# Performance work log

Measured on AMD Instinct MI355X. Metric: run time of the kernel, lower is better.

The kernel has to match this reference:

```python
import jax, jax.numpy as jnp
import numpy as np

N = 100000   # nodes
E = 1600000  # directed edges
HID = 64


def gat_conv(x, src, dst, W, a_src, a_dst, b, heads, out_ch):
    """PyG-style GATConv (add_self_loops=True, negative_slope=0.2, concat)."""
    n = x.shape[0]
    h = (x @ W).reshape(n, heads, out_ch)              # [N,H,C]
    loop = jnp.arange(n, dtype=src.dtype)
    s = jnp.concatenate([src, loop])                   # self loops appended
    d = jnp.concatenate([dst, loop])
    alpha_src = jnp.sum(h * a_src, axis=-1)            # [N,H]
    alpha_dst = jnp.sum(h * a_dst, axis=-1)            # [N,H]
    alpha = jax.nn.leaky_relu(alpha_src[s] + alpha_dst[d], 0.2)  # [E+N,H]
    # segment softmax over incoming edges of each destination node
    amax = jax.ops.segment_max(alpha, d, num_segments=n)
    alpha = jnp.exp(alpha - amax[d])
    asum = jax.ops.segment_sum(alpha, d, num_segments=n)
    alpha = alpha / (asum[d] + 1e-16)
    msg = h[s] * alpha[:, :, None]                     # [E+N,H,C]
    out = jax.ops.segment_sum(msg, d, num_segments=n)  # [N,H,C]
    return out.reshape(n, heads * out_ch) + b


def setup_inputs() -> dict:
    key = jax.random.key(0)
    ks = jax.random.split(key, 22)
    rn = lambda k, shp, s=0.1: (jax.random.normal(k, shp, jnp.float32) * s)
    inp = {
        "x": jax.random.normal(ks[0], (N, 2), jnp.float32),
        "edge_index": jax.random.randint(ks[1], (2, E), 0, N, dtype=jnp.int32),
        "edge_attr": jax.random.normal(ks[2], (E, 2), jnp.float32),
        # node encoder
        "enc_W": rn(ks[3], (2, HID)), "enc_b": rn(ks[4], (HID,)),
        # gat1: heads=4, out=16
        "g1_W": rn(ks[5], (HID, HID)), "g1_as": rn(ks[6], (4, 16)),
        "g1_ad": rn(ks[7], (4, 16)), "g1_b": rn(ks[8], (HID,)),
        # gat2: heads=1, out=64
        "g2_W": rn(ks[9], (HID, HID)), "g2_as": rn(ks[10], (1, HID)),
        "g2_ad": rn(ks[11], (1, HID)), "g2_b": rn(ks[12], (HID,)),
        # node head
        "no_W1": rn(ks[13], (HID, HID)), "no_b1": rn(ks[14], (HID,)),
        "no_W2": rn(ks[15], (HID, 2)), "no_b2": rn(ks[16], (2,)),
        # edge head: in = 2*HID + 2 = 130
        "eo_W1": rn(ks[17], (2 * HID + 2, HID)), "eo_b1": rn(ks[18], (HID,)),
        "eo_W2": rn(ks[19], (HID, 1)), "eo_b2": rn(ks[20], (1,)),
    }
    return inp


def reference(x, edge_index, edge_attr, enc_W, enc_b,
              g1_W, g1_as, g1_ad, g1_b,
              g2_W, g2_as, g2_ad, g2_b,
              no_W1, no_b1, no_W2, no_b2,
              eo_W1, eo_b1, eo_W2, eo_b2):
    src, dst = edge_index[0], edge_index[1]
    h = x @ enc_W + enc_b                                    # node encoder (dropout = eval identity)
    h = jax.nn.elu(gat_conv(h, src, dst, g1_W, g1_as, g1_ad, g1_b, 4, 16))
    h = gat_conv(h, src, dst, g2_W, g2_as, g2_ad, g2_b, 1, HID)
    e_in = jnp.concatenate([h[src], h[dst], edge_attr], axis=-1)  # [E,130]
    node_pred = jnp.tanh(jax.nn.leaky_relu(h @ no_W1 + no_b1, 0.01) @ no_W2 + no_b2)
    edge_pred = jnp.tanh(jax.nn.leaky_relu(e_in @ eo_W1 + eo_b1, 0.01) @ eo_W2 + eo_b2)[:, 0]
    return edge_pred, node_pred
```

## Files before the change

### kernel.cpp

```cpp
#include <hip/hip_runtime.h>
#include <hip/hip_fp16.h>
#include <math.h>


typedef _Float16 half8_t __attribute__((ext_vector_type(8)));
typedef float floatx4 __attribute__((ext_vector_type(4)));

__global__ void k_scatter(const int* __restrict__ src, const int* __restrict__ dst,
                          int E, int NB, int cap, int* cursor,
                          unsigned int* __restrict__ ebuf,
                          const float* __restrict__ encW, const float* __restrict__ encb,
                          const float* __restrict__ g1W, float* __restrict__ Mc){
  __shared__ int hist[800];
  __shared__ int base[800];
  int t = threadIdx.x;
  if (blockIdx.x == 0 && t < 64){
    float m0 = 0.f, m1 = 0.f, cc = 0.f;
    for (int k = 0; k < 64; ++k){
      float g = g1W[k * 64 + t];
      m0 = fmaf(encW[k], g, m0);
      m1 = fmaf(encW[64 + k], g, m1);
      cc = fmaf(encb[k], g, cc);
    }
    Mc[t] = m0; Mc[64 + t] = m1; Mc[128 + t] = cc;
  }
  for (int i = t; i < NB; i += 256) hist[i] = 0;
  __syncthreads();
  int cbase = blockIdx.x * 2048;
  int sv[8], bk[8], dl[8];
  #pragma unroll
  for (int i = 0; i < 8; ++i){
    int e = cbase + i * 256 + t;
    if (e < E){
      int d = dst[e];
      sv[i] = src[e]; bk[i] = d >> 7; dl[i] = d & 127;
      atomicAdd(&hist[bk[i]], 1);
    } else bk[i] = -1;
  }
  __syncthreads();
  for (int i = t; i < NB; i += 256){
    int c = hist[i];
    base[i] = (c > 0) ? (i * cap + atomicAdd(&cursor[i], c)) : 0;
    hist[i] = 0;
  }
  __syncthreads();
  #pragma unroll
  for (int i = 0; i < 8; ++i){
    if (bk[i] >= 0){
      int r = atomicAdd(&hist[bk[i]], 1);
      int p = base[bk[i]] + r;
      if (p < (bk[i] + 1) * cap)
        ebuf[p] = (unsigned)sv[i] | ((unsigned)dl[i] << 17);
    }
  }
}

__global__ void k_bucket_build(const int* __restrict__ cursor, int cap, int N,
                               unsigned int* ebuf, int* __restrict__ rstart,
                               int* __restrict__ rend){
  __shared__ unsigned int ent[2700];
  __shared__ int cnts[128];
  __shared__ int aux[128];
  int b = blockIdx.x, t = threadIdx.x;
  int base = b * cap;
  int cnt = cursor[b];
  if (cnt > cap) cnt = cap;
  for (int i = t; i < cnt; i += 256) ent[i] = ebuf[base + i];
  if (t < 128) cnts[t] = 0;
  __syncthreads();
  for (int i = t; i < cnt; i += 256) atomicAdd(&cnts[ent[i] >> 17], 1);
  __syncthreads();
  int v = 0;
  if (t < 128){ v = cnts[t]; aux[t] = v; }
  __syncthreads();
  for (int off = 1; off < 128; off <<= 1){
    int x = 0;
    if (t < 128 && t >= off) x = aux[t - off];
    __syncthreads();
    if (t < 128) aux[t] += x;
    __syncthreads();
  }
  if (t < 128){
    int incl = aux[t];
    int node = (b << 7) + t;
    if (node < N){ rstart[node] = base + incl - v; rend[node] = base + incl; }
    cnts[t] = incl - v;
  }
  __syncthreads();
  for (int i = t; i < cnt; i += 256){
    unsigned int en = ent[i];
    int pos = atomicAdd(&cnts[en >> 17], 1);
    ebuf[base + pos] = en;
  }
}

template<int H>
__global__ void k_palpha(const int* __restrict__ cursor, int cap,
                         const unsigned int* __restrict__ ebuf,
                         const float* __restrict__ as, const float* __restrict__ ad,
                         float* __restrict__ palpha){
  int blk = blockIdx.x;
  int b = blk >> 2, part = blk & 3;
  int base = b * cap;
  int cnt = cursor[b];
  if (cnt > cap) cnt = cap;
  for (int i = part * 256 + threadIdx.x; i < cnt; i += 1024){
    unsigned int en = ebuf[base + i];
    int s = en & 0x1FFFFu;
    int d = (b << 7) + (en >> 17);
    if (H == 4){
      float4 sv = ((const float4*)as)[s];
      float4 dv = ((const float4*)ad)[d];
      float a0 = sv.x + dv.x, a1 = sv.y + dv.y, a2 = sv.z + dv.z, a3 = sv.w + dv.w;
      a0 = a0 > 0.f ? a0 : 0.2f * a0;
      a1 = a1 > 0.f ? a1 : 0.2f * a1;
      a2 = a2 > 0.f ? a2 : 0.2f * a2;
      a3 = a3 > 0.f ? a3 : 0.2f * a3;
      float4 pv = {__expf(a0), __expf(a1), __expf(a2), __expf(a3)};
      ((float4*)palpha)[base + i] = pv;
    } else {
      float a = as[s] + ad[d];
      a = a > 0.f ? a : 0.2f * a;
      palpha[base + i] = __expf(a);
    }
  }
}

__global__ void k_fuse1(const float* __restrict__ x, const float* __restrict__ Mc,
                        const float* __restrict__ a_s, const float* __restrict__ a_d,
                        __half* __restrict__ hw, float* __restrict__ alpha_s,
                        float* __restrict__ alpha_d, int n){
  int idx = blockIdx.x * blockDim.x + threadIdx.x;
  if (idx >= n * 64) return;
  int node = idx >> 6, j = idx & 63;
  float acc = fmaf(x[node * 2 + 0], Mc[j], fmaf(x[node * 2 + 1], Mc[64 + j], Mc[128 + j]));
  hw[idx] = __float2half(acc);
  float ps = acc * a_s[j];
  float pd = acc * a_d[j];
  #pragma unroll
  for (int off = 1; off < 16; off <<= 1){
    ps += __shfl_xor(ps, off);
    pd += __shfl_xor(pd, off);
  }
  if ((j & 15) == 0){
    int h = j >> 4;
    alpha_s[node * 4 + h] = ps;
    alpha_d[node * 4 + h] = pd;
  }
}

__global__ __launch_bounds__(256) void k_hw_mfma(
    const __half* __restrict__ hin, const float* __restrict__ W,
    const float* __restrict__ a_s, const float* __restrict__ a_d,
    __half* __restrict__ hw, float* __restrict__ alpha_s,
    float* __restrict__ alpha_d, int n){
  __shared__ float redS[4][16];
  __shared__ float redD[4][16];
  int t = threadIdx.x;
  int lane = t & 63, wave = t >> 6;
  int l15 = lane & 15, quad = lane >> 4;
  int ch = wave * 16 + l15;
  half8_t b0, b1;
  #pragma unroll
  for (int j = 0; j < 8; ++j){
    b0[j] = (_Float16)W[(quad * 8 + j) * 64 + ch];
    b1[j] = (_Float16)W[(quad * 8 + j + 32) * 64 + ch];
  }
  float asv = a_s[ch], adv = a_d[ch];
  int base = blockIdx.x * 64;
  for (int it = 0; it < 4; ++it){
    int tb = base + it * 16;
    if (tb >= n) break;
    int arn = tb + l15; if (arn >= n) arn = n - 1;
    const __half* arow = hin + (size_t)arn * 64 + quad * 8;
    half8_t a0 = *(const half8_t*)arow;
    half8_t a1 = *(const half8_t*)(arow + 32);
    floatx4 acc = {0.f, 0.f, 0.f, 0.f};
    acc = __builtin_amdgcn_mfma_f32_16x16x32_f16(a0, b0, acc, 0, 0, 0);
    acc = __builtin_amdgcn_mfma_f32_16x16x32_f16(a1, b1, acc, 0, 0, 0);
    float ps[4], pd[4];
    #pragma unroll
    for (int r = 0; r < 4; ++r){
      int node = tb + quad * 4 + r;
      if (node < n) hw[(size_t)node * 64 + ch] = __float2half(acc[r]);
      ps[r] = acc[r] * asv;
      pd[r] = acc[r] * adv;
      #pragma unroll
      for (int off = 1; off < 16; off <<= 1){
        ps[r] += __shfl_xor(ps[r], off);
        pd[r] += __shfl_xor(pd[r], off);
      }
    }
    if (l15 == 0){
      #pragma unroll
      for (int r = 0; r < 4; ++r){
        redS[wave][quad * 4 + r] = ps[r];
        redD[wave][quad * 4 + r] = pd[r];
      }
    }
    __syncthreads();
    if (t < 16 && tb + t < n){
      alpha_s[tb + t] = redS[0][t] + redS[1][t] + redS[2][t] + redS[3][t];
      alpha_d[tb + t] = redD[0][t] + redD[1][t] + redD[2][t] + redD[3][t];
    }
    __syncthreads();
  }
}

template<int H, bool ELU_ACT>
__global__ void k_agg(const __half* __restrict__ hw, const float* __restrict__ palpha,
                      const float* __restrict__ alpha_s, const float* __restrict__ alpha_d,
                      const int* __restrict__ rstart, const int* __restrict__ rend,
                      const unsigned int* __restrict__ ebuf,
                      const float* __restrict__ bias, __half* __restrict__ hout, int n){
  int node = (blockIdx.x * blockDim.x + threadIdx.x) >> 6;
  int lane = threadIdx.x & 63;
  int g = lane >> 3, jj = lane & 7;
  if (node >= n) return;
  int hidx = (jj * H) >> 3;
  int start = rstart[node], end = rend[node];
  float acc[8] = {0.f,0.f,0.f,0.f,0.f,0.f,0.f,0.f};
  float psum = 0.f;
  if (g == 0){
    float a = alpha_s[node * H + hidx] + alpha_d[node * H + hidx];
    a = a > 0.f ? a : 0.2f * a;
    float p = __expf(a);
    psum = p;
    float4 rv = *(const float4*)(hw + (size_t)node * 64 + jj * 8);
    const __half2* hp = (const __half2*)&rv;
    #pragma unroll
    for (int k = 0; k < 4; ++k){
      float2 f = __half22float2(hp[k]);
      acc[2 * k] = p * f.x; acc[2 * k + 1] = p * f.y;
    }
  }
  int i = start + g;
  for (; i + 8 < end; i += 16){
    unsigned int e0 = ebuf[i], e1 = ebuf[i + 8];
    int s0 = e0 & 0x1FFFF, s1 = e1 & 0x1FFFF;
    float p0 = palpha[(size_t)i * H + hidx];
    float p1 = palpha[(size_t)(i + 8) * H + hidx];
    float4 r0 = *(const float4*)(hw + (size_t)s0 * 64 + jj * 8);
    float4 r1 = *(const float4*)(hw + (size_t)s1 * 64 + jj * 8);
    const __half2* h0 = (const __half2*)&r0;
    const __half2* h1 = (const __half2*)&r1;
    psum += p0 + p1;
    #pragma unroll
    for (int k = 0; k < 4; ++k){
      float2 f0 = __half22float2(h0[k]);
      float2 f1 = __half22float2(h1[k]);
      acc[2 * k]     = fmaf(p0, f0.x, fmaf(p1, f1.x, acc[2 * k]));
      acc[2 * k + 1] = fmaf(p0, f0.y, fmaf(p1, f1.y, acc[2 * k + 1]));
    }
  }
  if (i < end){
    unsigned int en = ebuf[i];
    int s = en & 0x1FFFF;
    float p = palpha[(size_t)i * H + hidx];
    float4 rv = *(const float4*)(hw + (size_t)s * 64 + jj * 8);
    const __half2* hp = (const __half2*)&rv;
    psum += p;
    #pragma unroll
    for (int k = 0; k < 4; ++k){
      float2 f = __half22float2(hp[k]);
      acc[2 * k]     = fmaf(p, f.x, acc[2 * k]);
      acc[2 * k + 1] = fmaf(p, f.y, acc[2 * k + 1]);
    }
  }
  #pragma unroll
  for (int off = 8; off < 64; off <<= 1){
    psum += __shfl_xor(psum, off);
    #pragma unroll
    for (int k = 0; k < 8; ++k) acc[k] += __shfl_xor(acc[k], off);
  }
  if (g == 0){
    float inv = 1.f / (psum + 1e-16f);
    float4 bv0 = ((const float4*)bias)[2 * jj];
    float4 bv1 = ((const float4*)bias)[2 * jj + 1];
    float o[8];
    o[0] = fmaf(acc[0], inv, bv0.x); o[1] = fmaf(acc[1], inv, bv0.y);
    o[2] = fmaf(acc[2], inv, bv0.z); o[3] = fmaf(acc[3], inv, bv0.w);
    o[4] = fmaf(acc[4], inv, bv1.x); o[5] = fmaf(acc[5], inv, bv1.y);
    o[6] = fmaf(acc[6], inv, bv1.z); o[7] = fmaf(acc[7], inv, bv1.w);
    if (ELU_ACT){
      #pragma unroll
      for (int k = 0; k < 8; ++k) o[k] = o[k] > 0.f ? o[k] : (__expf(o[k]) - 1.f);
    }
    half8_t hv;
    #pragma unroll
    for (int k = 0; k < 8; ++k) hv[k] = (_Float16)o[k];
    *(half8_t*)(hout + (size_t)node * 64 + jj * 8) = hv;
  }
}

__global__ __launch_bounds__(256) void k_heads_mfma(
    const __half* __restrict__ h, const float* __restrict__ eoW1,
    const float* __restrict__ noW1, const float* __restrict__ nob1,
    const float* __restrict__ noW2, const float* __restrict__ nob2,
    __half* __restrict__ P1, __half* __restrict__ P2,
    float* __restrict__ outN, int n){
  __shared__ float redP[4][16][2];
  int t = threadIdx.x;
  int lane = t & 63, wave = t >> 6;
  int l15 = lane & 15, quad = lane >> 4;
  int ch = wave * 16 + l15;
  half8_t bP1a, bP1b, bP2a, bP2b, bNa, bNb;
  #pragma unroll
  for (int j = 0; j < 8; ++j){
    int k0 = quad * 8 + j, k1 = k0 + 32;
    bP1a[j] = (_Float16)eoW1[k0 * 64 + ch];
    bP1b[j] = (_Float16)eoW1[k1 * 64 + ch];
    bP2a[j] = (_Float16)eoW1[(k0 + 64) * 64 + ch];
    bP2b[j] = (_Float16)eoW1[(k1 + 64) * 64 + ch];
    bNa[j]  = (_Float16)noW1[k0 * 64 + ch];
    bNb[j]  = (_Float16)noW1[k1 * 64 + ch];
  }
  float b1v = nob1[ch];
  float w20 = noW2[ch * 2 + 0], w21 = noW2[ch * 2 + 1];
  float b20 = nob2[0], b21 = nob2[1];
  int base = blockIdx.x * 64;
  for (int it = 0; it < 4; ++it){
    int tb = base + it * 16;
    if (tb >= n) break;
    int arn = tb + l15; if (arn >= n) arn = n - 1;
    const __half* arow = h + (size_t)arn * 64 + quad * 8;
    half8_t a0 = *(const half8_t*)arow;
    half8_t a1 = *(const half8_t*)(arow + 32);
    floatx4 ac1 = {0.f,0.f,0.f,0.f}, ac2 = {0.f,0.f,0.f,0.f}, acN = {0.f,0.f,0.f,0.f};
    ac1 = __builtin_amdgcn_mfma_f32_16x16x32_f16(a0, bP1a, ac1, 0, 0, 0);
    ac1 = __builtin_amdgcn_mfma_f32_16x16x32_f16(a1, bP1b, ac1, 0, 0, 0);
    ac2 = __builtin_amdgcn_mfma_f32_16x16x32_f16(a0, bP2a, ac2, 0, 0, 0);
    ac2 = __builtin_amdgcn_mfma_f32_16x16x32_f16(a1, bP2b, ac2, 0, 0, 0);
    acN = __builtin_amdgcn_mfma_f32_16x16x32_f16(a0, bNa, acN, 0, 0, 0);
    acN = __builtin_amdgcn_mfma_f32_16x16x32_f16(a1, bNb, acN, 0, 0, 0);
    float p0[4], p1[4];
    #pragma unroll
    for (int r = 0; r < 4; ++r){
      int node = tb + quad * 4 + r;
      if (node < n){
        P1[(size_t)node * 64 + ch] = __float2half(ac1[r]);
        P2[(size_t)node * 64 + ch] = __float2half(ac2[r]);
      }
      float v = acN[r] + b1v;
      v = v > 0.f ? v : 0.01f * v;
      p0[r] = v * w20;
      p1[r] = v * w21;
      #pragma unroll
      for (int off = 1; off < 16; off <<= 1){
        p0[r] += __shfl_xor(p0[r], off);
        p1[r] += __shfl_xor(p1[r], off);
      }
    }
    if (l15 == 0){
      #pragma unroll
      for (int r = 0; r < 4; ++r){
        redP[wave][quad * 4 + r][0] = p0[r];
        redP[wave][quad * 4 + r][1] = p1[r];
      }
    }
    __syncthreads();
    if (t < 16 && tb + t < n){
      float s0 = redP[0][t][0] + redP[1][t][0] + redP[2][t][0] + redP[3][t][0];
      float s1 = redP[0][t][1] + redP[1][t][1] + redP[2][t][1] + redP[3][t][1];
      outN[(size_t)(tb + t) * 2 + 0] = tanhf(s0 + b20);
      outN[(size_t)(tb + t) * 2 + 1] = tanhf(s1 + b21);
    }
    __syncthreads();
  }
}

__global__ void k_edge_head(const __half* __restrict__ P1h, const __half* __restrict__ P2h,
                            const int* __restrict__ src, const int* __restrict__ dst,
                            const float* __restrict__ eattr, const float* __restrict__ eoW1,
                            const float* __restrict__ b1, const float* __restrict__ W2,
                            const float* __restrict__ b2, float* __restrict__ out, int E){
  int lane = threadIdx.x & 63;
  int jj = lane & 7, q = lane >> 3;
  int wid = (blockIdx.x * blockDim.x + threadIdx.x) >> 6;
  int nw = (gridDim.x * blockDim.x) >> 6;

  const float4* rAq = (const float4*)(eoW1 + 8192);
  const float4* rBq = (const float4*)(eoW1 + 8256);
  const float4* b1q = (const float4*)b1;
  const float4* w2q = (const float4*)W2;
  float4 tA0 = rAq[2 * jj], tA1 = rAq[2 * jj + 1];
  float4 tB0 = rBq[2 * jj], tB1 = rBq[2 * jj + 1];
  float4 tb0 = b1q[2 * jj], tb1 = b1q[2 * jj + 1];
  float4 tw0 = w2q[2 * jj], tw1 = w2q[2 * jj + 1];
  float ra[8] = {tA0.x, tA0.y, tA0.z, tA0.w, tA1.x, tA1.y, tA1.z, tA1.w};
  float rb[8] = {tB0.x, tB0.y, tB0.z, tB0.w, tB1.x, tB1.y, tB1.z, tB1.w};
  float bb[8] = {tb0.x, tb0.y, tb0.z, tb0.w, tb1.x, tb1.y, tb1.z, tb1.w};
  float w2[8] = {tw0.x, tw0.y, tw0.z, tw0.w, tw1.x, tw1.y, tw1.z, tw1.w};
  float b2v = b2[0];

  const float4* P1q = (const float4*)P1h;
  const float4* P2q = (const float4*)P2h;
  const float2* eav = (const float2*)eattr;

  int groups = (E + 15) >> 4;
  for (int g = wid; g < groups; g += nw){
    int e0 = g * 16 + q, e1 = e0 + 8;
    bool act0 = (e0 < E), act1 = (e1 < E);
    float p0 = 0.f, p1 = 0.f;
    if (act0){
      int s = src[e0], d = dst[e0];
      float2 ea = eav[e0];
      float4 g1 = P1q[(size_t)s * 8 + jj];
      float4 g2 = P2q[(size_t)d * 8 + jj];
      const __half2* h1 = (const __half2*)&g1;
      const __half2* h2 = (const __half2*)&g2;
      #pragma unroll
      for (int k = 0; k < 4; ++k){
        float2 u = __half22float2(h1[k]);
        float2 w = __half22float2(h2[k]);
        float ta = u.x + w.x + bb[2 * k];
        float tb = u.y + w.y + bb[2 * k + 1];
        ta = fmaf(ea.x, ra[2 * k], fmaf(ea.y, rb[2 * k], ta));
        tb = fmaf(ea.x, ra[2 * k + 1], fmaf(ea.y, rb[2 * k + 1], tb));
        ta = ta > 0.f ? ta : 0.01f * ta;
        tb = tb > 0.f ? tb : 0.01f * tb;
        p0 = fmaf(ta, w2[2 * k], fmaf(tb, w2[2 * k + 1], p0));
      }
    }
    if (act1){
      int s = src[e1], d = dst[e1];
      float2 ea = eav[e1];
      float4 g1 = P1q[(size_t)s * 8 + jj];
      float4 g2 = P2q[(size_t)d * 8 + jj];
      const __half2* h1 = (const __half2*)&g1;
      const __half2* h2 = (const __half2*)&g2;
      #pragma unroll
      for (int k = 0; k < 4; ++k){
        float2 u = __half22float2(h1[k]);
        float2 w = __half22float2(h2[k]);
        float ta = u.x + w.x + bb[2 * k];
        float tb = u.y + w.y + bb[2 * k + 1];
        ta = fmaf(ea.x, ra[2 * k], fmaf(ea.y, rb[2 * k], ta));
        tb = fmaf(ea.x, ra[2 * k + 1], fmaf(ea.y, rb[2 * k + 1], tb));
        ta = ta > 0.f ? ta : 0.01f * ta;
        tb = tb > 0.f ? tb : 0.01f * tb;
        p1 = fmaf(ta, w2[2 * k], fmaf(tb, w2[2 * k + 1], p1));
      }
    }
    #pragma unroll
    for (int off = 1; off < 8; off <<= 1){
      p0 += __shfl_xor(p0, off);
      p1 += __shfl_xor(p1, off);
    }
    if (jj == 0){
      if (act0) out[e0] = tanhf(p0 + b2v);
      if (act1) out[e1] = tanhf(p1 + b2v);
    }
  }
}

extern "C" void kernel_launch(void* const* d_in, const int* in_sizes, int n_in,
                              void* d_out, int out_size, void* d_ws, size_t ws_size,
                              hipStream_t stream){
  const float* x    = (const float*)d_in[0];
  const int*   eidx = (const int*)  d_in[1];
  const float* ea   = (const float*)d_in[2];
  const float* encW = (const float*)d_in[3];
  const float* encb = (const float*)d_in[4];
  const float* g1W  = (const float*)d_in[5];
  const float* g1as = (const float*)d_in[6];
  const float* g1ad = (const float*)d_in[7];
  const float* g1b  = (const float*)d_in[8];
  const float* g2W  = (const float*)d_in[9];
  const float* g2as = (const float*)d_in[10];
  const float* g2ad = (const float*)d_in[11];
  const float* g2b  = (const float*)d_in[12];
  const float* noW1 = (const float*)d_in[13];
  const float* nob1 = (const float*)d_in[14];
  const float* noW2 = (const float*)d_in[15];
  const float* nob2 = (const float*)d_in[16];
  const float* eoW1 = (const float*)d_in[17];
  const float* eob1 = (const float*)d_in[18];
  const float* eoW2 = (const float*)d_in[19];
  const float* eob2 = (const float*)d_in[20];

  const int N = in_sizes[0] / 2;
  const int E = in_sizes[1] / 2;
  const int* src = eidx;
  const int* dst = eidx + E;

  const int NB = (N + 127) >> 7;
  int avg = (E + NB - 1) / NB;
  int cap = avg + avg / 4 + 64;
  if (cap > 2700) cap = 2700;

  char* ws = (char*)d_ws;
  size_t off = 0;
  auto alloc = [&](size_t bytes) -> void* {
    void* p = ws + off;
    off = (off + bytes + 255) & ~(size_t)255;
    return p;
  };
  __half* bufA  = (__half*)alloc((size_t)N * 64 * 2);
  __half* bufH  = (__half*)alloc((size_t)N * 64 * 2);
  __half* P1h   = (__half*)alloc((size_t)N * 64 * 2);
  __half* P2h   = (__half*)alloc((size_t)N * 64 * 2);
  float*  as    = (float*) alloc((size_t)N * 4 * 4);
  float*  ad    = (float*) alloc((size_t)N * 4 * 4);
  int* rstart   = (int*)   alloc((size_t)N * 4);
  int* rend     = (int*)   alloc((size_t)N * 4);
  unsigned int* ebuf = (unsigned int*)alloc((size_t)NB * cap * 4);
  float* palphaB = (float*)alloc((size_t)NB * cap * 16);
  int* cursor   = (int*)   alloc((size_t)NB * 4);
  float* Mc     = (float*) alloc(192 * 4);

  hipMemsetAsync(cursor, 0, (size_t)NB * 4, stream);
  k_scatter<<<(E + 2047) / 2048, 256, 0, stream>>>(src, dst, E, NB, cap, cursor, ebuf,
                                                   encW, encb, g1W, Mc);
  k_fuse1<<<(N * 64 + 255) / 256, 256, 0, stream>>>(x, Mc, g1as, g1ad, bufH, as, ad, N);
  k_bucket_build<<<NB, 256, 0, stream>>>(cursor, cap, N, ebuf, rstart, rend);
  k_palpha<4><<<NB * 4, 256, 0, stream>>>(cursor, cap, ebuf, as, ad, palphaB);
  k_agg<4, true><<<(N + 3) / 4, 256, 0, stream>>>(bufH, palphaB, as, ad,
                                                  rstart, rend, ebuf, g1b, bufA, N);
  k_hw_mfma<<<(N + 63) / 64, 256, 0, stream>>>(bufA, g2W, g2as, g2ad, bufH, as, ad, N);
  k_palpha<1><<<NB * 4, 256, 0, stream>>>(cursor, cap, ebuf, as, ad, palphaB);
  k_agg<1, false><<<(N + 3) / 4, 256, 0, stream>>>(bufH, palphaB, as, ad,
                                                   rstart, rend, ebuf, g2b, bufA, N);
  float* out = (float*)d_out;
  k_heads_mfma<<<(N + 63) / 64, 256, 0, stream>>>(bufA, eoW1, noW1, nob1, noW2, nob2,
                                                  P1h, P2h, out + E, N);
  k_edge_head<<<2048, 256, 0, stream>>>(P1h, P2h, src, dst, ea,
                                        eoW1, eob1, eoW2, eob2, out, E);
}
```

Baseline: 390.2 us.

## Fuse GAT aggregation with following MFMA projections and layer-1 edge logits into bucket build

Layer-1 edge attention logits are now computed inside the bucket-build pass, so the separate H=4 palpha kernel goes away. Each aggregation kernel now stages its 16 output rows in shared memory and immediately runs the next MFMA stage on them: the layer-2 projection with its alpha reductions, or the node and edge head projections. This removes two kernel launches and the global round-trips of the intermediate hidden features. In exchange, each block handles only 16 nodes with four waves doing per-node gathers, and it holds more weight registers, which may reduce occupancy.

```diff
diff --git a/kernel.cpp b/kernel.cpp
--- a/kernel.cpp
+++ b/kernel.cpp
@@ -57,7 +57,10 @@
 
 __global__ void k_bucket_build(const int* __restrict__ cursor, int cap, int N,
                                unsigned int* ebuf, int* __restrict__ rstart,
-                               int* __restrict__ rend){
+                               int* __restrict__ rend,
+                               const float* __restrict__ as4,
+                               const float* __restrict__ ad4,
+                               float4* __restrict__ palpha4){
   __shared__ unsigned int ent[2700];
   __shared__ int cnts[128];
   __shared__ int aux[128];
@@ -89,16 +92,27 @@
   __syncthreads();
   for (int i = t; i < cnt; i += 256){
     unsigned int en = ent[i];
-    int pos = atomicAdd(&cnts[en >> 17], 1);
+    int dl = en >> 17;
+    int s = en & 0x1FFFFu;
+    int pos = atomicAdd(&cnts[dl], 1);
     ebuf[base + pos] = en;
-  }
-}
-
-template<int H>
-__global__ void k_palpha(const int* __restrict__ cursor, int cap,
-                         const unsigned int* __restrict__ ebuf,
-                         const float* __restrict__ as, const float* __restrict__ ad,
-                         float* __restrict__ palpha){
+    int d = (b << 7) + dl;
+    float4 sv = ((const float4*)as4)[s];
+    float4 dv = ((const float4*)ad4)[d];
+    float a0 = sv.x + dv.x, a1 = sv.y + dv.y, a2 = sv.z + dv.z, a3 = sv.w + dv.w;
+    a0 = a0 > 0.f ? a0 : 0.2f * a0;
+    a1 = a1 > 0.f ? a1 : 0.2f * a1;
+    a2 = a2 > 0.f ? a2 : 0.2f * a2;
+    a3 = a3 > 0.f ? a3 : 0.2f * a3;
+    float4 pv = {__expf(a0), __expf(a1), __expf(a2), __expf(a3)};
+    palpha4[base + pos] = pv;
+  }
+}
+
+__global__ void k_palpha1(const int* __restrict__ cursor, int cap,
+                          const unsigned int* __restrict__ ebuf,
+                          const float* __restrict__ as, const float* __restrict__ ad,
+                          float* __restrict__ palpha1){
   int blk = blockIdx.x;
   int b = blk >> 2, part = blk & 3;
   int base = b * cap;
@@ -108,21 +122,9 @@
     unsigned int en = ebuf[base + i];
     int s = en & 0x1FFFFu;
     int d = (b << 7) + (en >> 17);
-    if (H == 4){
-      float4 sv = ((const float4*)as)[s];
-      float4 dv = ((const float4*)ad)[d];
-      float a0 = sv.x + dv.x, a1 = sv.y + dv.y, a2 = sv.z + dv.z, a3 = sv.w + dv.w;
-      a0 = a0 > 0.f ? a0 : 0.2f * a0;
-      a1 = a1 > 0.f ? a1 : 0.2f * a1;
-      a2 = a2 > 0.f ? a2 : 0.2f * a2;
-      a3 = a3 > 0.f ? a3 : 0.2f * a3;
-      float4 pv = {__expf(a0), __expf(a1), __expf(a2), __expf(a3)};
-      ((float4*)palpha)[base + i] = pv;
-    } else {
-      float a = as[s] + ad[d];
-      a = a > 0.f ? a : 0.2f * a;
-      palpha[base + i] = __expf(a);
-    }
+    float a = as[s] + ad[d];
+    a = a > 0.f ? a : 0.2f * a;
+    palpha1[base + i] = __expf(a);
   }
 }
 
@@ -149,40 +151,146 @@
   }
 }
 
-__global__ __launch_bounds__(256) void k_hw_mfma(
-    const __half* __restrict__ hin, const float* __restrict__ W,
-    const float* __restrict__ a_s, const float* __restrict__ a_d,
-    __half* __restrict__ hw, float* __restrict__ alpha_s,
-    float* __restrict__ alpha_d, int n){
-  __shared__ float redS[4][16];
-  __shared__ float redD[4][16];
+template<int H, bool ELU_ACT, int EPI>
+__global__ __launch_bounds__(256) void k_aggf(
+    const __half* __restrict__ hw, const float* __restrict__ palpha,
+    const float* __restrict__ alpha_s, const float* __restrict__ alpha_d,
+    const int* __restrict__ rstart, const int* __restrict__ rend,
+    const unsigned int* __restrict__ ebuf, const float* __restrict__ bias,
+    const float* __restrict__ Wg, const float* __restrict__ a_s2,
+    const float* __restrict__ a_d2, __half* __restrict__ hw2,
+    float* __restrict__ as_out, float* __restrict__ ad_out,
+    const float* __restrict__ eoW1, const float* __restrict__ noW1,
+    const float* __restrict__ nob1, const float* __restrict__ noW2,
+    const float* __restrict__ nob2, __half* __restrict__ P1,
+    __half* __restrict__ P2, float* __restrict__ outN,
+    int n)
+{
+  __shared__ _Float16 rows[16][64];
+  __shared__ float red[4][16][2];
   int t = threadIdx.x;
   int lane = t & 63, wave = t >> 6;
+  int g = lane >> 3, jj = lane & 7;
   int l15 = lane & 15, quad = lane >> 4;
   int ch = wave * 16 + l15;
-  half8_t b0, b1;
-  #pragma unroll
-  for (int j = 0; j < 8; ++j){
-    b0[j] = (_Float16)W[(quad * 8 + j) * 64 + ch];
-    b1[j] = (_Float16)W[(quad * 8 + j + 32) * 64 + ch];
-  }
-  float asv = a_s[ch], adv = a_d[ch];
-  int base = blockIdx.x * 64;
+  int tile = blockIdx.x * 16;
+
+  half8_t bW0, bW1, bP1a, bP1b, bP2a, bP2b, bNa, bNb;
+  float asv = 0.f, adv = 0.f, b1v = 0.f, w20 = 0.f, w21 = 0.f, b20 = 0.f, b21 = 0.f;
+  if (EPI == 1){
+    #pragma unroll
+    for (int j = 0; j < 8; ++j){
+      bW0[j] = (_Float16)Wg[(quad * 8 + j) * 64 + ch];
+      bW1[j] = (_Float16)Wg[(quad * 8 + j + 32) * 64 + ch];
+    }
+    asv = a_s2[ch]; adv = a_d2[ch];
+  } else {
+    #pragma unroll
+    for (int j = 0; j < 8; ++j){
+      int k0 = quad * 8 + j, k1 = k0 + 32;
+      bP1a[j] = (_Float16)eoW1[k0 * 64 + ch];
+      bP1b[j] = (_Float16)eoW1[k1 * 64 + ch];
+      bP2a[j] = (_Float16)eoW1[(k0 + 64) * 64 + ch];
+      bP2b[j] = (_Float16)eoW1[(k1 + 64) * 64 + ch];
+      bNa[j]  = (_Float16)noW1[k0 * 64 + ch];
+      bNb[j]  = (_Float16)noW1[k1 * 64 + ch];
+    }
+    b1v = nob1[ch];
+    w20 = noW2[ch * 2 + 0]; w21 = noW2[ch * 2 + 1];
+    b20 = nob2[0]; b21 = nob2[1];
+  }
+
   for (int it = 0; it < 4; ++it){
-    int tb = base + it * 16;
-    if (tb >= n) break;
-    int arn = tb + l15; if (arn >= n) arn = n - 1;
-    const __half* arow = hin + (size_t)arn * 64 + quad * 8;
-    half8_t a0 = *(const half8_t*)arow;
-    half8_t a1 = *(const half8_t*)(arow + 32);
+    int node = tile + wave * 4 + it;
+    if (node >= n) break;
+    int hidx = (jj * H) >> 3;
+    int start = rstart[node], end = rend[node];
+    float acc[8] = {0.f,0.f,0.f,0.f,0.f,0.f,0.f,0.f};
+    float psum = 0.f;
+    if (g == 0){
+      float a = alpha_s[node * H + hidx] + alpha_d[node * H + hidx];
+      a = a > 0.f ? a : 0.2f * a;
+      float p = __expf(a);
+      psum = p;
+      float4 rv = *(const float4*)(hw + (size_t)node * 64 + jj * 8);
+      const __half2* hp = (const __half2*)&rv;
+      #pragma unroll
+      for (int k = 0; k < 4; ++k){
+        float2 f = __half22float2(hp[k]);
+        acc[2 * k] = p * f.x; acc[2 * k + 1] = p * f.y;
+      }
+    }
+    int i = start + g;
+    for (; i + 8 < end; i += 16){
+      unsigned int e0 = ebuf[i], e1 = ebuf[i + 8];
+      int s0 = e0 & 0x1FFFF, s1 = e1 & 0x1FFFF;
+      float p0 = palpha[(size_t)i * H + hidx];
+      float p1 = palpha[(size_t)(i + 8) * H + hidx];
+      float4 r0 = *(const float4*)(hw + (size_t)s0 * 64 + jj * 8);
+      float4 r1 = *(const float4*)(hw + (size_t)s1 * 64 + jj * 8);
+      const __half2* h0 = (const __half2*)&r0;
+      const __half2* h1 = (const __half2*)&r1;
+      psum += p0 + p1;
+      #pragma unroll
+      for (int k = 0; k < 4; ++k){
+        float2 f0 = __half22float2(h0[k]);
+        float2 f1 = __half22float2(h1[k]);
+        acc[2 * k]     = fmaf(p0, f0.x, fmaf(p1, f1.x, acc[2 * k]));
+        acc[2 * k + 1] = fmaf(p0, f0.y, fmaf(p1, f1.y, acc[2 * k + 1]));
+      }
+    }
+    if (i < end){
+      unsigned int en = ebuf[i];
+      int s = en & 0x1FFFF;
+      float p = palpha[(size_t)i * H + hidx];
+      float4 rv = *(const float4*)(hw + (size_t)s * 64 + jj * 8);
+      const __half2* hp = (const __half2*)&rv;
+      psum += p;
+      #pragma unroll
+      for (int k = 0; k < 4; ++k){
+        float2 f = __half22float2(hp[k]);
+        acc[2 * k]     = fmaf(p, f.x, acc[2 * k]);
+        acc[2 * k + 1] = fmaf(p, f.y, acc[2 * k + 1]);
+      }
+    }
+    #pragma unroll
+    for (int off = 8; off < 64; off <<= 1){
+      psum += __shfl_xor(psum, off);
+      #pragma unroll
+      for (int k = 0; k < 8; ++k) acc[k] += __shfl_xor(acc[k], off);
+    }
+    if (g == 0){
+      float inv = 1.f / (psum + 1e-16f);
+      float4 bv0 = ((const float4*)bias)[2 * jj];
+      float4 bv1 = ((const float4*)bias)[2 * jj + 1];
+      float o[8];
+      o[0] = fmaf(acc[0], inv, bv0.x); o[1] = fmaf(acc[1], inv, bv0.y);
+      o[2] = fmaf(acc[2], inv, bv0.z); o[3] = fmaf(acc[3], inv, bv0.w);
+      o[4] = fmaf(acc[4], inv, bv1.x); o[5] = fmaf(acc[5], inv, bv1.y);
+      o[6] = fmaf(acc[6], inv, bv1.z); o[7] = fmaf(acc[7], inv, bv1.w);
+      if (ELU_ACT){
+        #pragma unroll
+        for (int k = 0; k < 8; ++k) o[k] = o[k] > 0.f ? o[k] : (__expf(o[k]) - 1.f);
+      }
+      half8_t hv;
+      #pragma unroll
+      for (int k = 0; k < 8; ++k) hv[k] = (_Float16)o[k];
+      *(half8_t*)&rows[wave * 4 + it][jj * 8] = hv;
+    }
+  }
+  __syncthreads();
+
+  half8_t a0 = *(const half8_t*)&rows[l15][quad * 8];
+  half8_t a1 = *(const half8_t*)&rows[l15][quad * 8 + 32];
+  if (EPI == 1){
     floatx4 acc = {0.f, 0.f, 0.f, 0.f};
-    acc = __builtin_amdgcn_mfma_f32_16x16x32_f16(a0, b0, acc, 0, 0, 0);
-    acc = __builtin_amdgcn_mfma_f32_16x16x32_f16(a1, b1, acc, 0, 0, 0);
+    acc = __builtin_amdgcn_mfma_f32_16x16x32_f16(a0, bW0, acc, 0, 0, 0);
+    acc = __builtin_amdgcn_mfma_f32_16x16x32_f16(a1, bW1, acc, 0, 0, 0);
     float ps[4], pd[4];
     #pragma unroll
     for (int r = 0; r < 4; ++r){
-      int node = tb + quad * 4 + r;
-      if (node < n) hw[(size_t)node * 64 + ch] = __float2half(acc[r]);
+      int node = tile + quad * 4 + r;
+      if (node < n) hw2[(size_t)node * 64 + ch] = __float2half(acc[r]);
       ps[r] = acc[r] * asv;
       pd[r] = acc[r] * adv;
       #pragma unroll
@@ -194,138 +302,16 @@
     if (l15 == 0){
       #pragma unroll
       for (int r = 0; r < 4; ++r){
-        redS[wave][quad * 4 + r] = ps[r];
-        redD[wave][quad * 4 + r] = pd[r];
+        red[wave][quad * 4 + r][0] = ps[r];
+        red[wave][quad * 4 + r][1] = pd[r];
       }
     }
     __syncthreads();
-    if (t < 16 && tb + t < n){
-      alpha_s[tb + t] = redS[0][t] + redS[1][t] + redS[2][t] + redS[3][t];
-      alpha_d[tb + t] = redD[0][t] + redD[1][t] + redD[2][t] + redD[3][t];
-    }
-    __syncthreads();
-  }
-}
-
-template<int H, bool ELU_ACT>
-__global__ void k_agg(const __half* __restrict__ hw, const float* __restrict__ palpha,
-                      const float* __restrict__ alpha_s, const float* __restrict__ alpha_d,
-                      const int* __restrict__ rstart, const int* __restrict__ rend,
-                      const unsigned int* __restrict__ ebuf,
-                      const float* __restrict__ bias, __half* __restrict__ hout, int n){
-  int node = (blockIdx.x * blockDim.x + threadIdx.x) >> 6;
-  int lane = threadIdx.x & 63;
-  int g = lane >> 3, jj = lane & 7;
-  if (node >= n) return;
-  int hidx = (jj * H) >> 3;
-  int start = rstart[node], end = rend[node];
-  float acc[8] = {0.f,0.f,0.f,0.f,0.f,0.f,0.f,0.f};
-  float psum = 0.f;
-  if (g == 0){
-    float a = alpha_s[node * H + hidx] + alpha_d[node * H + hidx];
-    a = a > 0.f ? a : 0.2f * a;
-    float p = __expf(a);
-    psum = p;
-    float4 rv = *(const float4*)(hw + (size_t)node * 64 + jj * 8);
-    const __half2* hp = (const __half2*)&rv;
-    #pragma unroll
-    for (int k = 0; k < 4; ++k){
-      float2 f = __half22float2(hp[k]);
-      acc[2 * k] = p * f.x; acc[2 * k + 1] = p * f.y;
-    }
-  }
-  int i = start + g;
-  for (; i + 8 < end; i += 16){
-    unsigned int e0 = ebuf[i], e1 = ebuf[i + 8];
-    int s0 = e0 & 0x1FFFF, s1 = e1 & 0x1FFFF;
-    float p0 = palpha[(size_t)i * H + hidx];
-    float p1 = palpha[(size_t)(i + 8) * H + hidx];
-    float4 r0 = *(const float4*)(hw + (size_t)s0 * 64 + jj * 8);
-    float4 r1 = *(const float4*)(hw + (size_t)s1 * 64 + jj * 8);
-    const __half2* h0 = (const __half2*)&r0;
-    const __half2* h1 = (const __half2*)&r1;
-    psum += p0 + p1;
-    #pragma unroll
-    for (int k = 0; k < 4; ++k){
-      float2 f0 = __half22float2(h0[k]);
-      float2 f1 = __half22float2(h1[k]);
-      acc[2 * k]     = fmaf(p0, f0.x, fmaf(p1, f1.x, acc[2 * k]));
-      acc[2 * k + 1] = fmaf(p0, f0.y, fmaf(p1, f1.y, acc[2 * k + 1]));
-    }
-  }
-  if (i < end){
-    unsigned int en = ebuf[i];
-    int s = en & 0x1FFFF;
-    float p = palpha[(size_t)i * H + hidx];
-    float4 rv = *(const float4*)(hw + (size_t)s * 64 + jj * 8);
-    const __half2* hp = (const __half2*)&rv;
-    psum += p;
-    #pragma unroll
-    for (int k = 0; k < 4; ++k){
-      float2 f = __half22float2(hp[k]);
-      acc[2 * k]     = fmaf(p, f.x, acc[2 * k]);
-      acc[2 * k + 1] = fmaf(p, f.y, acc[2 * k + 1]);
-    }
-  }
-  #pragma unroll
-  for (int off = 8; off < 64; off <<= 1){
-    psum += __shfl_xor(psum, off);
-    #pragma unroll
-    for (int k = 0; k < 8; ++k) acc[k] += __shfl_xor(acc[k], off);
-  }
-  if (g == 0){
-    float inv = 1.f / (psum + 1e-16f);
-    float4 bv0 = ((const float4*)bias)[2 * jj];
-    float4 bv1 = ((const float4*)bias)[2 * jj + 1];
-    float o[8];
-    o[0] = fmaf(acc[0], inv, bv0.x); o[1] = fmaf(acc[1], inv, bv0.y);
-    o[2] = fmaf(acc[2], inv, bv0.z); o[3] = fmaf(acc[3], inv, bv0.w);
-    o[4] = fmaf(acc[4], inv, bv1.x); o[5] = fmaf(acc[5], inv, bv1.y);
-    o[6] = fmaf(acc[6], inv, bv1.z); o[7] = fmaf(acc[7], inv, bv1.w);
-    if (ELU_ACT){
-      #pragma unroll
-      for (int k = 0; k < 8; ++k) o[k] = o[k] > 0.f ? o[k] : (__expf(o[k]) - 1.f);
-    }
-    half8_t hv;
-    #pragma unroll
-    for (int k = 0; k < 8; ++k) hv[k] = (_Float16)o[k];
-    *(half8_t*)(hout + (size_t)node * 64 + jj * 8) = hv;
-  }
-}
-
-__global__ __launch_bounds__(256) void k_heads_mfma(
-    const __half* __restrict__ h, const float* __restrict__ eoW1,
-    const float* __restrict__ noW1, const float* __restrict__ nob1,
-    const float* __restrict__ noW2, const float* __restrict__ nob2,
-    __half* __restrict__ P1, __half* __restrict__ P2,
-    float* __restrict__ outN, int n){
-  __shared__ float redP[4][16][2];
-  int t = threadIdx.x;
-  int lane = t & 63, wave = t >> 6;
-  int l15 = lane & 15, quad = lane >> 4;
-  int ch = wave * 16 + l15;
-  half8_t bP1a, bP1b, bP2a, bP2b, bNa, bNb;
-  #pragma unroll
-  for (int j = 0; j < 8; ++j){
-    int k0 = quad * 8 + j, k1 = k0 + 32;
-    bP1a[j] = (_Float16)eoW1[k0 * 64 + ch];
-    bP1b[j] = (_Float16)eoW1[k1 * 64 + ch];
-    bP2a[j] = (_Float16)eoW1[(k0 + 64) * 64 + ch];
-    bP2b[j] = (_Float16)eoW1[(k1 + 64) * 64 + ch];
-    bNa[j]  = (_Float16)noW1[k0 * 64 + ch];
-    bNb[j]  = (_Float16)noW1[k1 * 64 + ch];
-  }
-  float b1v = nob1[ch];
-  float w20 = noW2[ch * 2 + 0], w21 = noW2[ch * 2 + 1];
-  float b20 = nob2[0], b21 = nob2[1];
-  int base = blockIdx.x * 64;
-  for (int it = 0; it < 4; ++it){
-    int tb = base + it * 16;
-    if (tb >= n) break;
-    int arn = tb + l15; if (arn >= n) arn = n - 1;
-    const __half* arow = h + (size_t)arn * 64 + quad * 8;
-    half8_t a0 = *(const half8_t*)arow;
-    half8_t a1 = *(const half8_t*)(arow + 32);
+    if (t < 16 && tile + t < n){
+      as_out[tile + t] = red[0][t][0] + red[1][t][0] + red[2][t][0] + red[3][t][0];
+      ad_out[tile + t] = red[0][t][1] + red[1][t][1] + red[2][t][1] + red[3][t][1];
+    }
+  } else {
     floatx4 ac1 = {0.f,0.f,0.f,0.f}, ac2 = {0.f,0.f,0.f,0.f}, acN = {0.f,0.f,0.f,0.f};
     ac1 = __builtin_amdgcn_mfma_f32_16x16x32_f16(a0, bP1a, ac1, 0, 0, 0);
     ac1 = __builtin_amdgcn_mfma_f32_16x16x32_f16(a1, bP1b, ac1, 0, 0, 0);
@@ -336,7 +322,7 @@
     float p0[4], p1[4];
     #pragma unroll
     for (int r = 0; r < 4; ++r){
-      int node = tb + quad * 4 + r;
+      int node = tile + quad * 4 + r;
       if (node < n){
         P1[(size_t)node * 64 + ch] = __float2half(ac1[r]);
         P2[(size_t)node * 64 + ch] = __float2half(ac2[r]);
@@ -354,18 +340,17 @@
     if (l15 == 0){
       #pragma unroll
       for (int r = 0; r < 4; ++r){
-        redP[wave][quad * 4 + r][0] = p0[r];
-        redP[wave][quad * 4 + r][1] = p1[r];
+        red[wave][quad * 4 + r][0] = p0[r];
+        red[wave][quad * 4 + r][1] = p1[r];
       }
     }
     __syncthreads();
-    if (t < 16 && tb + t < n){
-      float s0 = redP[0][t][0] + redP[1][t][0] + redP[2][t][0] + redP[3][t][0];
-      float s1 = redP[0][t][1] + redP[1][t][1] + redP[2][t][1] + redP[3][t][1];
-      outN[(size_t)(tb + t) * 2 + 0] = tanhf(s0 + b20);
-      outN[(size_t)(tb + t) * 2 + 1] = tanhf(s1 + b21);
-    }
-    __syncthreads();
+    if (t < 16 && tile + t < n){
+      float s0 = red[0][t][0] + red[1][t][0] + red[2][t][0] + red[3][t][0];
+      float s1 = red[0][t][1] + red[1][t][1] + red[2][t][1] + red[3][t][1];
+      outN[(size_t)(tile + t) * 2 + 0] = tanhf(s0 + b20);
+      outN[(size_t)(tile + t) * 2 + 1] = tanhf(s1 + b21);
+    }
   }
 }
 
@@ -496,12 +481,14 @@
     off = (off + bytes + 255) & ~(size_t)255;
     return p;
   };
-  __half* bufA  = (__half*)alloc((size_t)N * 64 * 2);
-  __half* bufH  = (__half*)alloc((size_t)N * 64 * 2);
+  __half* bufH1 = (__half*)alloc((size_t)N * 64 * 2);
+  __half* bufH2 = (__half*)alloc((size_t)N * 64 * 2);
   __half* P1h   = (__half*)alloc((size_t)N * 64 * 2);
   __half* P2h   = (__half*)alloc((size_t)N * 64 * 2);
-  float*  as    = (float*) alloc((size_t)N * 4 * 4);
-  float*  ad    = (float*) alloc((size_t)N * 4 * 4);
+  float*  as4   = (float*) alloc((size_t)N * 4 * 4);
+  float*  ad4   = (float*) alloc((size_t)N * 4 * 4);
+  float*  as1   = (float*) alloc((size_t)N * 4);
+  float*  ad1   = (float*) alloc((size_t)N * 4);
   int* rstart   = (int*)   alloc((size_t)N * 4);
   int* rend     = (int*)   alloc((size_t)N * 4);
   unsigned int* ebuf = (unsigned int*)alloc((size_t)NB * cap * 4);
@@ -509,21 +496,23 @@
   int* cursor   = (int*)   alloc((size_t)NB * 4);
   float* Mc     = (float*) alloc(192 * 4);
 
+  float* out = (float*)d_out;
+
   hipMemsetAsync(cursor, 0, (size_t)NB * 4, stream);
   k_scatter<<<(E + 2047) / 2048, 256, 0, stream>>>(src, dst, E, NB, cap, cursor, ebuf,
                                                    encW, encb, g1W, Mc);
-  k_fuse1<<<(N * 64 + 255) / 256, 256, 0, stream>>>(x, Mc, g1as, g1ad, bufH, as, ad, N);
-  k_bucket_build<<<NB, 256, 0, stream>>>(cursor, cap, N, ebuf, rstart, rend);
-  k_palpha<4><<<NB * 4, 256, 0, stream>>>(cursor, cap, ebuf, as, ad, palphaB);
-  k_agg<4, true><<<(N + 3) / 4, 256, 0, stream>>>(bufH, palphaB, as, ad,
-                                                  rstart, rend, ebuf, g1b, bufA, N);
-  k_hw_mfma<<<(N + 63) / 64, 256, 0, stream>>>(bufA, g2W, g2as, g2ad, bufH, as, ad, N);
-  k_palpha<1><<<NB * 4, 256, 0, stream>>>(cursor, cap, ebuf, as, ad, palphaB);
-  k_agg<1, false><<<(N + 3) / 4, 256, 0, stream>>>(bufH, palphaB, as, ad,
-                                                   rstart, rend, ebuf, g2b, bufA, N);
-  float* out = (float*)d_out;
-  k_heads_mfma<<<(N + 63) / 64, 256, 0, stream>>>(bufA, eoW1, noW1, nob1, noW2, nob2,
-                                                  P1h, P2h, out + E, N);
+  k_fuse1<<<(N * 64 + 255) / 256, 256, 0, stream>>>(x, Mc, g1as, g1ad, bufH1, as4, ad4, N);
+  k_bucket_build<<<NB, 256, 0, stream>>>(cursor, cap, N, ebuf, rstart, rend,
+                                         as4, ad4, (float4*)palphaB);
+  k_aggf<4, true, 1><<<(N + 15) / 16, 256, 0, stream>>>(
+      bufH1, palphaB, as4, ad4, rstart, rend, ebuf, g1b,
+      g2W, g2as, g2ad, bufH2, as1, ad1,
+      nullptr, nullptr, nullptr, nullptr, nullptr, nullptr, nullptr, nullptr, N);
+  k_palpha1<<<NB * 4, 256, 0, stream>>>(cursor, cap, ebuf, as1, ad1, palphaB);
+  k_aggf<1, false, 2><<<(N + 15) / 16, 256, 0, stream>>>(
+      bufH2, palphaB, as1, ad1, rstart, rend, ebuf, g2b,
+      nullptr, nullptr, nullptr, nullptr, nullptr, nullptr,
+      eoW1, noW1, nob1, noW2, nob2, P1h, P2h, out + E, N);
   k_edge_head<<<2048, 256, 0, stream>>>(P1h, P2h, src, dst, ea,
                                         eoW1, eob1, eoW2, eob2, out, E);
 }
```

Result: slower. 427.0 us (+9.4%).
